# Performance work log

Hardware: AMD Instinct MI355X
Metric: run time of the kernel (lower is better)

The kernel has to match this reference:

```python
import jax, jax.numpy as jnp
import numpy as np

EPS = 1e-5
NEG_SLOPE = 0.01


def _bn(h, gamma, beta):
    # Training-mode batch norm over axis 0 (biased variance, like torch)
    m = h.mean(axis=0)
    v = h.var(axis=0)
    return (h - m) * jax.lax.rsqrt(v + EPS) * gamma + beta


def setup_inputs() -> dict:
    N, F, H, C = 2048, 64, 128, 2
    key = jax.random.key(0)
    ks = jax.random.split(key, 12)
    g = lambda k, shp: jax.random.normal(k, shp, dtype=jnp.float32) * 0.05
    return {
        "x": jax.random.normal(ks[0], (N, F), dtype=jnp.float32),
        "node_features": jax.random.uniform(ks[1], (N, F), dtype=jnp.float32),
        "W1": g(ks[2], (F, H)), "b1": jnp.zeros((H,), jnp.float32),
        "g1": jnp.ones((H,), jnp.float32), "be1": jnp.zeros((H,), jnp.float32),
        "W2": g(ks[3], (H, H)), "b2": jnp.zeros((H,), jnp.float32),
        "g2": jnp.ones((H,), jnp.float32), "be2": jnp.zeros((H,), jnp.float32),
        "W3": g(ks[4], (H, F)), "b3": jnp.zeros((F,), jnp.float32),
        "W5": g(ks[5], (F, H)), "b5": jnp.zeros((H,), jnp.float32),
        "g5": jnp.ones((H,), jnp.float32), "be5": jnp.zeros((H,), jnp.float32),
        "W6": g(ks[6], (H, C)), "b6": jnp.zeros((C,), jnp.float32),
    }


def reference(x, node_features, W1, b1, g1, be1, W2, b2, g2, be2, W3, b3,
              W5, b5, g5, be5, W6, b6):
    N = node_features.shape[0]
    C = W6.shape[1]
    # static upper-triangular edge list == torch.combinations(arange(N), r=2)
    ei, ej = np.triu_indices(N, k=1)

    h = node_features
    xinit = h
    h = _bn(jax.nn.leaky_relu(h @ W1 + b1, NEG_SLOPE), g1, be1)
    h = _bn(jax.nn.leaky_relu(h @ W2 + b2, NEG_SLOPE), g2, be2)
    h = h @ W3 + b3 + xinit  # [N, F]

    # edge prediction: gather pairs, elementwise mult, MLP+BN+softmax
    e = h[ei] * h[ej]  # [E, F]
    e = _bn(jax.nn.leaky_relu(e @ W5 + b5, NEG_SLOPE), g5, be5)
    edge_pred = jax.nn.softmax(e @ W6 + b6, axis=-1)  # [E, C]

    probs = jnp.zeros((N, N, C), dtype=edge_pred.dtype)
    probs = probs.at[ei, ej].set(edge_pred).at[ej, ei].set(edge_pred)
    return probs
```

## Files before the change

kernel.cpp:

```cpp
#include <hip/hip_runtime.h>
#include <hip/hip_bf16.h>


typedef short short8 __attribute__((ext_vector_type(8)));
typedef float floatx4 __attribute__((ext_vector_type(4)));
typedef float float2v __attribute__((ext_vector_type(2)));

#define NN 2048
#define EPSV 1e-5f
#define EDGEF 2096128.f

__device__ __forceinline__ float bf2f(short s) {
    return __uint_as_float(((unsigned)(unsigned short)s) << 16);
}
__device__ __forceinline__ short f2bf(float f) {
    unsigned u = __float_as_uint(f);
    unsigned r = (u + 0x7FFFu + ((u >> 16) & 1u)) >> 16;
    return (short)r;
}
__device__ __forceinline__ float lrelu(float x) { return fmaxf(x, 0.01f * x); }

__device__ __forceinline__ unsigned cvt_pk_bf16(float a, float b) {
    unsigned r;
    asm("v_cvt_pk_bf16_f32 %0, %1, %2" : "=v"(r) : "v"(a), "v"(b));
    return r;
}

__device__ __forceinline__ int physB(int h, int f) {
    return ((((h >> 4) * 2 + (f >> 5)) * 64 + ((f >> 3) & 3) * 16 + (h & 15)) * 8) + (f & 7);
}

__device__ __forceinline__ void decode2(int bid, int& i0, int& j0, bool& str) {
    int q = (int)(0.25f * (130.f - sqrtf(16900.f - 8.f * (float)bid)));
    if (q < 0) q = 0;
    while (q > 0 && 130 * q - 2 * q * q > bid) --q;
    while (130 * (q + 1) - 2 * (q + 1) * (q + 1) <= bid) ++q;
    int r = bid - (130 * q - 2 * q * q);
    int n = 32 - q;
    int gs = (r >= n) + (r >= 2 * n) + (r >= 3 * n);
    int g = 4 * q + gs;
    int s = r - gs * n;
    i0 = g * 16;
    j0 = (q + s) * 64;
    str = (s == 0);
}

__global__ __launch_bounds__(256) void k_l1(const float* __restrict__ nf,
                                            const float* __restrict__ W1,
                                            const float* __restrict__ b1,
                                            const float* __restrict__ W5,
                                            float* __restrict__ act1,
                                            float* __restrict__ stat1,
                                            short* __restrict__ w5bf) {
    __shared__ float xl[8 * 64];
    __shared__ float sS[128], sQ[128];
    int t = threadIdx.x, n0 = blockIdx.x * 8;
    if (blockIdx.x < 32) {
        int idx = blockIdx.x * 256 + t;
        w5bf[physB(idx & 127, idx >> 7)] = f2bf(W5[idx]);
    }
    if (t < 128) { sS[t] = 0.f; sQ[t] = 0.f; }
    xl[t] = nf[(size_t)n0 * 64 + t];
    xl[t + 256] = nf[(size_t)n0 * 64 + t + 256];
    __syncthreads();
    int nl = t >> 5, h0 = (t & 31) * 4;
    float acc[4];
    for (int k = 0; k < 4; ++k) acc[k] = b1[h0 + k];
    for (int f = 0; f < 64; ++f) {
        float r = xl[nl * 64 + f];
        const float* wr = W1 + f * 128 + h0;
        for (int k = 0; k < 4; ++k) acc[k] = fmaf(r, wr[k], acc[k]);
    }
    for (int k = 0; k < 4; ++k) {
        float a = lrelu(acc[k]);
        act1[(size_t)(n0 + nl) * 128 + h0 + k] = a;
        atomicAdd(&sS[h0 + k], a);
        atomicAdd(&sQ[h0 + k], a * a);
    }
    __syncthreads();
    if (t < 128) atomicAdd(&stat1[t], sS[t]);
    else atomicAdd(&stat1[t], sQ[t - 128]);
}

__global__ __launch_bounds__(256) void k_l2(const float* __restrict__ act1,
                                            const float* __restrict__ stat1,
                                            const float* __restrict__ g1,
                                            const float* __restrict__ be1,
                                            const float* __restrict__ W2,
                                            const float* __restrict__ b2,
                                            float* __restrict__ act2,
                                            float* __restrict__ stat2) {
    __shared__ float a1n[8 * 128];
    __shared__ float sS[128], sQ[128];
    int t = threadIdx.x, n0 = blockIdx.x * 8;
    if (t < 128) { sS[t] = 0.f; sQ[t] = 0.f; }
    for (int k = 0; k < 4; ++k) {
        int e = t + 256 * k;
        int nl = e >> 7, h = e & 127;
        float m = stat1[h] * (1.f / 2048.f);
        float v = stat1[128 + h] * (1.f / 2048.f) - m * m;
        float sc = rsqrtf(v + EPSV);
        a1n[e] = (act1[(size_t)(n0 + nl) * 128 + h] - m) * sc * g1[h] + be1[h];
    }
    __syncthreads();
    int nl = t >> 5, h0 = (t & 31) * 4;
    float acc[4];
    for (int k = 0; k < 4; ++k) acc[k] = b2[h0 + k];
    for (int hi = 0; hi < 128; ++hi) {
        float r = a1n[nl * 128 + hi];
        const float* wr = W2 + hi * 128 + h0;
        for (int k = 0; k < 4; ++k) acc[k] = fmaf(r, wr[k], acc[k]);
    }
    for (int k = 0; k < 4; ++k) {
        float a = lrelu(acc[k]);
        act2[(size_t)(n0 + nl) * 128 + h0 + k] = a;
        atomicAdd(&sS[h0 + k], a);
        atomicAdd(&sQ[h0 + k], a * a);
    }
    __syncthreads();
    if (t < 128) atomicAdd(&stat2[t], sS[t]);
    else atomicAdd(&stat2[t], sQ[t - 128]);
}

__global__ __launch_bounds__(256) void k_l3(const float* __restrict__ act2,
                                            const float* __restrict__ stat2,
                                            const float* __restrict__ g2,
                                            const float* __restrict__ be2,
                                            const float* __restrict__ W3,
                                            const float* __restrict__ b3,
                                            const float* __restrict__ nf,
                                            short* __restrict__ hb,
                                            float* __restrict__ hf) {
    __shared__ float a2n[8 * 128];
    int t = threadIdx.x, n0 = blockIdx.x * 8;
    for (int k = 0; k < 4; ++k) {
        int e = t + 256 * k;
        int nl = e >> 7, h = e & 127;
        float m = stat2[h] * (1.f / 2048.f);
        float v = stat2[128 + h] * (1.f / 2048.f) - m * m;
        float sc = rsqrtf(v + EPSV);
        a2n[e] = (act2[(size_t)(n0 + nl) * 128 + h] - m) * sc * g2[h] + be2[h];
    }
    __syncthreads();
    int nl = t >> 5, f0 = (t & 31) * 2;
    float acc[2] = {0.f, 0.f};
    for (int hi = 0; hi < 128; ++hi) {
        float r = a2n[nl * 128 + hi];
        const float* wr = W3 + hi * 64 + f0;
        acc[0] = fmaf(r, wr[0], acc[0]);
        acc[1] = fmaf(r, wr[1], acc[1]);
    }
    float v0 = acc[0] + b3[f0] + nf[(size_t)(n0 + nl) * 64 + f0];
    float v1 = acc[1] + b3[f0 + 1] + nf[(size_t)(n0 + nl) * 64 + f0 + 1];
    unsigned p = (unsigned)(unsigned short)f2bf(v0) |
                 ((unsigned)(unsigned short)f2bf(v1) << 16);
    ((unsigned*)hb)[(size_t)(n0 + nl) * 32 + (f0 >> 1)] = p;
    hf[(size_t)(n0 + nl) * 64 + f0] = v0;
    hf[(size_t)(n0 + nl) * 64 + f0 + 1] = v1;
}

__global__ void k_mid(const float* __restrict__ SQe8, const float* __restrict__ W6,
                      const float* __restrict__ b6, const float* __restrict__ g5,
                      const float* __restrict__ be5, float* __restrict__ w6d,
                      float* __restrict__ b6d) {
    __shared__ float part[128];
    int h = threadIdx.x;
    float s = 0.f, q = 0.f;
    for (int x = 0; x < 8; ++x) {
        s += SQe8[x * 256 + h];
        q += SQe8[x * 256 + 128 + h];
    }
    float m = s / EDGEF;
    float v = q / EDGEF - m * m;
    float sc = rsqrtf(v + EPSV);
    float dW = W6[h * 2] - W6[h * 2 + 1];
    float sg = sc * g5[h];
    w6d[h] = sg * dW;
    part[h] = (be5[h] - m * sg) * dW;
    __syncthreads();
    if (h == 0) {
        float acc = b6[0] - b6[1];
        for (int k = 0; k < 128; ++k) acc += part[k];
        b6d[0] = acc;
    }
}

__global__ __launch_bounds__(256, 3) void edge_p1(
    const short* __restrict__ hb, const float* __restrict__ hf,
    const short* __restrict__ w5bf, const float* __restrict__ b5,
    float* __restrict__ SQe8)
{
    __shared__ __align__(16) float hi[16 * 64];
    int i0, j0; bool str;
    decode2(blockIdx.x, i0, j0, str);
    int t = threadIdx.x, lane = t & 63, w = t >> 6;
    int quad = lane >> 4, col = lane & 15;

    ((float4*)hi)[t] = ((const float4*)(hf + (size_t)i0 * 64))[t];

    float hjf[2][8];
#pragma unroll
    for (int ks = 0; ks < 2; ++ks) {
        short8 hv = *(const short8*)(hb + (size_t)(j0 + w * 16 + col) * 64 + ks * 32 + quad * 8);
#pragma unroll
        for (int e = 0; e < 8; ++e) hjf[ks][e] = bf2f(hv[e]);
    }
    short8 w5f[8][2];
#pragma unroll
    for (int n = 0; n < 8; ++n)
#pragma unroll
        for (int ks = 0; ks < 2; ++ks)
            w5f[n][ks] = ((const short8*)w5bf)[(n * 2 + ks) * 64 + lane];
    float b5v[8];
#pragma unroll
    for (int n = 0; n < 8; ++n) b5v[n] = b5[n * 16 + col];

    float S[8], Q[8];
#pragma unroll
    for (int n = 0; n < 8; ++n) { S[n] = 0.f; Q[n] = 0.f; }
    floatx4 zero4 = {0.f, 0.f, 0.f, 0.f};

    __syncthreads();

    auto mkfrag = [&](int il, short8 (&af)[2]) {
#pragma unroll
        for (int ks = 0; ks < 2; ++ks) {
            const float* hp = &hi[il * 64 + ks * 32 + quad * 8];
            float4 h0 = *(const float4*)hp;
            float4 h1 = *(const float4*)(hp + 4);
            int4 aw;
            aw.x = cvt_pk_bf16(h0.x * hjf[ks][0], h0.y * hjf[ks][1]);
            aw.y = cvt_pk_bf16(h0.z * hjf[ks][2], h0.w * hjf[ks][3]);
            aw.z = cvt_pk_bf16(h1.x * hjf[ks][4], h1.y * hjf[ks][5]);
            aw.w = cvt_pk_bf16(h1.z * hjf[ks][6], h1.w * hjf[ks][7]);
            af[ks] = *(short8*)&aw;
        }
    };

    if (!str) {
#pragma unroll 2
        for (int il = 0; il < 16; ++il) {
            short8 af[2];
            mkfrag(il, af);
#pragma unroll
            for (int n = 0; n < 8; ++n) {
                floatx4 c = __builtin_amdgcn_mfma_f32_16x16x32_bf16(af[0], w5f[n][0], zero4, 0, 0, 0);
                c = __builtin_amdgcn_mfma_f32_16x16x32_bf16(af[1], w5f[n][1], c, 0, 0, 0);
                float b = b5v[n];
#pragma unroll
                for (int r = 0; r < 4; ++r) {
                    float a = lrelu(c[r] + b);
                    S[n] += a;
                    Q[n] = fmaf(a, a, Q[n]);
                }
            }
        }
    } else {
        int jgb = j0 + w * 16 + quad * 4;
#pragma unroll 2
        for (int il = 0; il < 16; ++il) {
            short8 af[2];
            mkfrag(il, af);
            int ig = i0 + il;
#pragma unroll
            for (int n = 0; n < 8; ++n) {
                floatx4 c = __builtin_amdgcn_mfma_f32_16x16x32_bf16(af[0], w5f[n][0], zero4, 0, 0, 0);
                c = __builtin_amdgcn_mfma_f32_16x16x32_bf16(af[1], w5f[n][1], c, 0, 0, 0);
                float b = b5v[n];
#pragma unroll
                for (int r = 0; r < 4; ++r) {
                    float a = (jgb + r > ig) ? lrelu(c[r] + b) : 0.f;
                    S[n] += a;
                    Q[n] = fmaf(a, a, Q[n]);
                }
            }
        }
    }

    float* dst = SQe8 + (blockIdx.x & 7) * 256;
#pragma unroll
    for (int n = 0; n < 8; ++n) {
        float Sa = S[n], Qa = Q[n];
        Sa += __shfl_xor(Sa, 16); Sa += __shfl_xor(Sa, 32);
        Qa += __shfl_xor(Qa, 16); Qa += __shfl_xor(Qa, 32);
        if (quad == 0) {
            atomicAdd(&dst[n * 16 + col], Sa);
            atomicAdd(&dst[128 + n * 16 + col], Qa);
        }
    }
}

__global__ __launch_bounds__(256, 3) void edge_p2(
    const short* __restrict__ hb, const float* __restrict__ hf,
    const short* __restrict__ w5bf, const float* __restrict__ b5,
    const float* __restrict__ w6d, const float* __restrict__ b6dp,
    float* __restrict__ out)
{
    __shared__ __align__(16) float hi[16 * 64];
    __shared__ float sp[16][65];
    int i0, j0; bool str;
    decode2(blockIdx.x, i0, j0, str);
    int t = threadIdx.x, lane = t & 63, w = t >> 6;
    int quad = lane >> 4, col = lane & 15;

    ((float4*)hi)[t] = ((const float4*)(hf + (size_t)i0 * 64))[t];

    float hjf[2][8];
#pragma unroll
    for (int ks = 0; ks < 2; ++ks) {
        short8 hv = *(const short8*)(hb + (size_t)(j0 + w * 16 + col) * 64 + ks * 32 + quad * 8);
#pragma unroll
        for (int e = 0; e < 8; ++e) hjf[ks][e] = bf2f(hv[e]);
    }
    short8 w5f[8][2];
#pragma unroll
    for (int n = 0; n < 8; ++n)
#pragma unroll
        for (int ks = 0; ks < 2; ++ks)
            w5f[n][ks] = ((const short8*)w5bf)[(n * 2 + ks) * 64 + lane];
    float b5v[8], w6v[8];
#pragma unroll
    for (int n = 0; n < 8; ++n) {
        b5v[n] = b5[n * 16 + col];
        w6v[n] = w6d[n * 16 + col];
    }
    float bb = b6dp[0];
    floatx4 zero4 = {0.f, 0.f, 0.f, 0.f};

    __syncthreads();

    auto mkfrag = [&](int il, short8 (&af)[2]) {
#pragma unroll
        for (int ks = 0; ks < 2; ++ks) {
            const float* hp = &hi[il * 64 + ks * 32 + quad * 8];
            float4 h0 = *(const float4*)hp;
            float4 h1 = *(const float4*)(hp + 4);
            int4 aw;
            aw.x = cvt_pk_bf16(h0.x * hjf[ks][0], h0.y * hjf[ks][1]);
            aw.y = cvt_pk_bf16(h0.z * hjf[ks][2], h0.w * hjf[ks][3]);
            aw.z = cvt_pk_bf16(h1.x * hjf[ks][4], h1.y * hjf[ks][5]);
            aw.w = cvt_pk_bf16(h1.z * hjf[ks][6], h1.w * hjf[ks][7]);
            af[ks] = *(short8*)&aw;
        }
    };

#pragma unroll 2
    for (int il = 0; il < 16; ++il) {
        short8 af[2];
        mkfrag(il, af);
        float acc[4] = {0.f, 0.f, 0.f, 0.f};
#pragma unroll
        for (int n = 0; n < 8; ++n) {
            floatx4 c = __builtin_amdgcn_mfma_f32_16x16x32_bf16(af[0], w5f[n][0], zero4, 0, 0, 0);
            c = __builtin_amdgcn_mfma_f32_16x16x32_bf16(af[1], w5f[n][1], c, 0, 0, 0);
            float b = b5v[n], wv = w6v[n];
#pragma unroll
            for (int r = 0; r < 4; ++r)
                acc[r] = fmaf(lrelu(c[r] + b), wv, acc[r]);
        }
#pragma unroll
        for (int d = 1; d < 16; d <<= 1)
#pragma unroll
            for (int r = 0; r < 4; ++r) acc[r] += __shfl_xor(acc[r], d);
        if (col == 0) {
#pragma unroll
            for (int r = 0; r < 4; ++r) {
                float v = acc[r] + bb;
                sp[il][w * 16 + quad * 4 + r] = 1.f / (1.f + __expf(-v));
            }
        }
    }
    __syncthreads();

    if (!str) {
        int il = t >> 4, jb = (t & 15) * 4;
        float* op = out + ((size_t)(i0 + il) * NN + j0 + jb) * 2;
#pragma unroll
        for (int q2 = 0; q2 < 2; ++q2) {
            float p0 = sp[il][jb + q2 * 2], p1 = sp[il][jb + q2 * 2 + 1];
            float4 u; u.x = p0; u.y = 1.f - p0; u.z = p1; u.w = 1.f - p1;
            *(float4*)(op + q2 * 4) = u;
        }
        int jl = t >> 2, ib = (t & 3) * 4;
        float* om = out + ((size_t)(j0 + jl) * NN + i0 + ib) * 2;
#pragma unroll
        for (int q2 = 0; q2 < 2; ++q2) {
            float p0 = sp[ib + q2 * 2][jl], p1 = sp[ib + q2 * 2 + 1][jl];
            float4 u; u.x = p0; u.y = 1.f - p0; u.z = p1; u.w = 1.f - p1;
            *(float4*)(om + q2 * 4) = u;
        }
    } else {
        int il = t >> 4, jb = (t & 15) * 4;
        int ig = i0 + il;
#pragma unroll
        for (int e = 0; e < 4; ++e) {
            int jg = j0 + jb + e;
            if (jg > ig) {
                float p = sp[il][jb + e];
                float2v pr; pr.x = p; pr.y = 1.f - p;
                *(float2v*)(out + ((size_t)ig * NN + jg) * 2) = pr;
            } else if (jg == ig) {
                float2v pr; pr.x = 0.f; pr.y = 0.f;
                *(float2v*)(out + ((size_t)ig * NN + jg) * 2) = pr;
            }
        }
        int jl = t >> 2, ib = (t & 3) * 4;
        int jg = j0 + jl;
#pragma unroll
        for (int e = 0; e < 4; ++e) {
            int ig2 = i0 + ib + e;
            if (jg > ig2) {
                float p = sp[ib + e][jl];
                float2v pr; pr.x = p; pr.y = 1.f - p;
                *(float2v*)(out + ((size_t)jg * NN + ig2) * 2) = pr;
            }
        }
    }
}

extern "C" void kernel_launch(void* const* d_in, const int* in_sizes, int n_in,
                              void* d_out, int out_size, void* d_ws, size_t ws_size,
                              hipStream_t stream) {
    const float* nf  = (const float*)d_in[1];
    const float* W1  = (const float*)d_in[2];
    const float* b1  = (const float*)d_in[3];
    const float* g1  = (const float*)d_in[4];
    const float* be1 = (const float*)d_in[5];
    const float* W2  = (const float*)d_in[6];
    const float* b2  = (const float*)d_in[7];
    const float* g2  = (const float*)d_in[8];
    const float* be2 = (const float*)d_in[9];
    const float* W3  = (const float*)d_in[10];
    const float* b3  = (const float*)d_in[11];
    const float* W5  = (const float*)d_in[12];
    const float* b5  = (const float*)d_in[13];
    const float* g5  = (const float*)d_in[14];
    const float* be5 = (const float*)d_in[15];
    const float* W6  = (const float*)d_in[16];
    const float* b6  = (const float*)d_in[17];
    float* out = (float*)d_out;

    float* wsf   = (float*)d_ws;
    float* stat1 = wsf;
    float* stat2 = wsf + 256;
    float* SQe8  = wsf + 512;
    float* w6d   = wsf + 2560;
    float* b6dp  = wsf + 2688;
    float* act1  = wsf + 4096;
    float* act2  = act1 + 262144;
    short* hb    = (short*)(act2 + 262144);
    short* w5bf  = hb + 131072;
    float* hf    = (float*)(w5bf + 8192);

    hipMemsetAsync(d_ws, 0, 4096 * sizeof(float), stream);

    k_l1<<<256, 256, 0, stream>>>(nf, W1, b1, W5, act1, stat1, w5bf);
    k_l2<<<256, 256, 0, stream>>>(act1, stat1, g1, be1, W2, b2, act2, stat2);
    k_l3<<<256, 256, 0, stream>>>(act2, stat2, g2, be2, W3, b3, nf, hb, hf);

    edge_p1<<<2112, 256, 0, stream>>>(hb, hf, w5bf, b5, SQe8);
    k_mid<<<1, 128, 0, stream>>>(SQe8, W6, b6, g5, be5, w6d, b6dp);
    edge_p2<<<2112, 256, 0, stream>>>(hb, hf, w5bf, b5, w6d, b6dp, out);
}
```

Measured before the change: 251.9 us.

## Fuse BN-stat finalize into edge_p2, fold bias into MFMA, transpose output reduction

Removes the single-block k_mid launch by having every edge_p2 block recompute the folded BN5/W6 coefficients from the partial sums, reducing them with wave shuffles and shared memory. In both edge kernels the bias b5 now initialises the MFMA accumulator, so the separate bias add is gone. edge_p2 swaps the MFMA operands so each lane's four accumulator rows map to hidden units; the W6 dot then reduces with two cross-quad shuffles instead of four shuffles per row. Launch bounds go from 3 to 4 waves per SIMD, which adds register pressure, and each block redoes a small amount of redundant stats work.

```diff
diff --git a/kernel.cpp b/kernel.cpp
--- a/kernel.cpp
+++ b/kernel.cpp
@@ -159,33 +159,7 @@
     hf[(size_t)(n0 + nl) * 64 + f0 + 1] = v1;
 }
 
-__global__ void k_mid(const float* __restrict__ SQe8, const float* __restrict__ W6,
-                      const float* __restrict__ b6, const float* __restrict__ g5,
-                      const float* __restrict__ be5, float* __restrict__ w6d,
-                      float* __restrict__ b6d) {
-    __shared__ float part[128];
-    int h = threadIdx.x;
-    float s = 0.f, q = 0.f;
-    for (int x = 0; x < 8; ++x) {
-        s += SQe8[x * 256 + h];
-        q += SQe8[x * 256 + 128 + h];
-    }
-    float m = s / EDGEF;
-    float v = q / EDGEF - m * m;
-    float sc = rsqrtf(v + EPSV);
-    float dW = W6[h * 2] - W6[h * 2 + 1];
-    float sg = sc * g5[h];
-    w6d[h] = sg * dW;
-    part[h] = (be5[h] - m * sg) * dW;
-    __syncthreads();
-    if (h == 0) {
-        float acc = b6[0] - b6[1];
-        for (int k = 0; k < 128; ++k) acc += part[k];
-        b6d[0] = acc;
-    }
-}
-
-__global__ __launch_bounds__(256, 3) void edge_p1(
+__global__ __launch_bounds__(256, 4) void edge_p1(
     const short* __restrict__ hb, const float* __restrict__ hf,
     const short* __restrict__ w5bf, const float* __restrict__ b5,
     float* __restrict__ SQe8)
@@ -218,7 +192,6 @@
     float S[8], Q[8];
 #pragma unroll
     for (int n = 0; n < 8; ++n) { S[n] = 0.f; Q[n] = 0.f; }
-    floatx4 zero4 = {0.f, 0.f, 0.f, 0.f};
 
     __syncthreads();
 
@@ -244,12 +217,13 @@
             mkfrag(il, af);
 #pragma unroll
             for (int n = 0; n < 8; ++n) {
-                floatx4 c = __builtin_amdgcn_mfma_f32_16x16x32_bf16(af[0], w5f[n][0], zero4, 0, 0, 0);
+                float b = b5v[n];
+                floatx4 c = {b, b, b, b};
+                c = __builtin_amdgcn_mfma_f32_16x16x32_bf16(af[0], w5f[n][0], c, 0, 0, 0);
                 c = __builtin_amdgcn_mfma_f32_16x16x32_bf16(af[1], w5f[n][1], c, 0, 0, 0);
-                float b = b5v[n];
 #pragma unroll
                 for (int r = 0; r < 4; ++r) {
-                    float a = lrelu(c[r] + b);
+                    float a = lrelu(c[r]);
                     S[n] += a;
                     Q[n] = fmaf(a, a, Q[n]);
                 }
@@ -264,12 +238,13 @@
             int ig = i0 + il;
 #pragma unroll
             for (int n = 0; n < 8; ++n) {
-                floatx4 c = __builtin_amdgcn_mfma_f32_16x16x32_bf16(af[0], w5f[n][0], zero4, 0, 0, 0);
+                float b = b5v[n];
+                floatx4 c = {b, b, b, b};
+                c = __builtin_amdgcn_mfma_f32_16x16x32_bf16(af[0], w5f[n][0], c, 0, 0, 0);
                 c = __builtin_amdgcn_mfma_f32_16x16x32_bf16(af[1], w5f[n][1], c, 0, 0, 0);
-                float b = b5v[n];
 #pragma unroll
                 for (int r = 0; r < 4; ++r) {
-                    float a = (jgb + r > ig) ? lrelu(c[r] + b) : 0.f;
+                    float a = (jgb + r > ig) ? lrelu(c[r]) : 0.f;
                     S[n] += a;
                     Q[n] = fmaf(a, a, Q[n]);
                 }
@@ -290,13 +265,16 @@
     }
 }
 
-__global__ __launch_bounds__(256, 3) void edge_p2(
+__global__ __launch_bounds__(256, 4) void edge_p2(
     const short* __restrict__ hb, const float* __restrict__ hf,
     const short* __restrict__ w5bf, const float* __restrict__ b5,
-    const float* __restrict__ w6d, const float* __restrict__ b6dp,
-    float* __restrict__ out)
+    const float* __restrict__ SQe8, const float* __restrict__ W6,
+    const float* __restrict__ b6, const float* __restrict__ g5,
+    const float* __restrict__ be5, float* __restrict__ out)
 {
     __shared__ __align__(16) float hi[16 * 64];
+    __shared__ __align__(16) float sw6[128];
+    __shared__ float sred[2];
     __shared__ float sp[16][65];
     int i0, j0; bool str;
     decode2(blockIdx.x, i0, j0, str);
@@ -305,6 +283,26 @@
 
     ((float4*)hi)[t] = ((const float4*)(hf + (size_t)i0 * 64))[t];
 
+    float partv = 0.f;
+    if (t < 128) {
+        float s = 0.f, q = 0.f;
+#pragma unroll
+        for (int x = 0; x < 8; ++x) {
+            s += SQe8[x * 256 + t];
+            q += SQe8[x * 256 + 128 + t];
+        }
+        float m = s * (1.f / EDGEF);
+        float v = q * (1.f / EDGEF) - m * m;
+        float sc = rsqrtf(v + EPSV);
+        float dW = W6[t * 2] - W6[t * 2 + 1];
+        float sg = sc * g5[t];
+        sw6[t] = sg * dW;
+        partv = (be5[t] - m * sg) * dW;
+    }
+#pragma unroll
+    for (int d = 1; d < 64; d <<= 1) partv += __shfl_xor(partv, d);
+    if (t < 128 && lane == 0) sred[w] = partv;
+
     float hjf[2][8];
 #pragma unroll
     for (int ks = 0; ks < 2; ++ks) {
@@ -318,16 +316,17 @@
 #pragma unroll
         for (int ks = 0; ks < 2; ++ks)
             w5f[n][ks] = ((const short8*)w5bf)[(n * 2 + ks) * 64 + lane];
-    float b5v[8], w6v[8];
-#pragma unroll
-    for (int n = 0; n < 8; ++n) {
-        b5v[n] = b5[n * 16 + col];
-        w6v[n] = w6d[n * 16 + col];
-    }
-    float bb = b6dp[0];
-    floatx4 zero4 = {0.f, 0.f, 0.f, 0.f};
-
-    __syncthreads();
+    floatx4 b5q4[8];
+#pragma unroll
+    for (int n = 0; n < 8; ++n)
+        b5q4[n] = *(const floatx4*)(b5 + n * 16 + quad * 4);
+
+    __syncthreads();
+    float bb = b6[0] - b6[1] + sred[0] + sred[1];
+    floatx4 w6q4[8];
+#pragma unroll
+    for (int n = 0; n < 8; ++n)
+        w6q4[n] = *(const floatx4*)&sw6[n * 16 + quad * 4];
 
     auto mkfrag = [&](int il, short8 (&af)[2]) {
 #pragma unroll
@@ -348,27 +347,21 @@
     for (int il = 0; il < 16; ++il) {
         short8 af[2];
         mkfrag(il, af);
-        float acc[4] = {0.f, 0.f, 0.f, 0.f};
+        float va[4] = {0.f, 0.f, 0.f, 0.f};
 #pragma unroll
         for (int n = 0; n < 8; ++n) {
-            floatx4 c = __builtin_amdgcn_mfma_f32_16x16x32_bf16(af[0], w5f[n][0], zero4, 0, 0, 0);
-            c = __builtin_amdgcn_mfma_f32_16x16x32_bf16(af[1], w5f[n][1], c, 0, 0, 0);
-            float b = b5v[n], wv = w6v[n];
+            floatx4 c = __builtin_amdgcn_mfma_f32_16x16x32_bf16(w5f[n][0], af[0], b5q4[n], 0, 0, 0);
+            c = __builtin_amdgcn_mfma_f32_16x16x32_bf16(w5f[n][1], af[1], c, 0, 0, 0);
 #pragma unroll
             for (int r = 0; r < 4; ++r)
-                acc[r] = fmaf(lrelu(c[r] + b), wv, acc[r]);
-        }
-#pragma unroll
-        for (int d = 1; d < 16; d <<= 1)
-#pragma unroll
-            for (int r = 0; r < 4; ++r) acc[r] += __shfl_xor(acc[r], d);
-        if (col == 0) {
-#pragma unroll
-            for (int r = 0; r < 4; ++r) {
-                float v = acc[r] + bb;
-                sp[il][w * 16 + quad * 4 + r] = 1.f / (1.f + __expf(-v));
-            }
-        }
+                va[r] = fmaf(lrelu(c[r]), ((const float*)&w6q4[n])[r], va[r]);
+        }
+        float v = (va[0] + va[1]) + (va[2] + va[3]);
+        v += __shfl_xor(v, 16);
+        v += __shfl_xor(v, 32);
+        v += bb;
+        float p = 1.f / (1.f + __expf(-v));
+        if (quad == 0) sp[il][w * 16 + col] = p;
     }
     __syncthreads();
 
@@ -444,8 +437,6 @@
     float* stat1 = wsf;
     float* stat2 = wsf + 256;
     float* SQe8  = wsf + 512;
-    float* w6d   = wsf + 2560;
-    float* b6dp  = wsf + 2688;
     float* act1  = wsf + 4096;
     float* act2  = act1 + 262144;
     short* hb    = (short*)(act2 + 262144);
@@ -459,6 +450,5 @@
     k_l3<<<256, 256, 0, stream>>>(act2, stat2, g2, be2, W3, b3, nf, hb, hf);
 
     edge_p1<<<2112, 256, 0, stream>>>(hb, hf, w5bf, b5, SQe8);
-    k_mid<<<1, 128, 0, stream>>>(SQe8, W6, b6, g5, be5, w6d, b6dp);
-    edge_p2<<<2112, 256, 0, stream>>>(hb, hf, w5bf, b5, w6d, b6dp, out);
-}
+    edge_p2<<<2112, 256, 0, stream>>>(hb, hf, w5bf, b5, SQe8, W6, b6, g5, be5, out);
+}
```

New measurement: 675.0 us. 168% more time.
